# Kernel optimization log

Measured on AMD Instinct MI355X. Metric: run time of the kernel, lower is better.

Reference implementation:

```python
import jax, jax.numpy as jnp
import numpy as np

KERNELS = (2, 4, 8, 16, 32)
DICE_EPS = 1e-6
WEIGHT = 1.0


def _projections(x):
    # x: [B, D, H, W] foreground volume. Three axis-max projections, each [B, 128, 128].
    return jnp.stack([x.max(axis=3),   # axial:    max over W -> [B, D, H]
                      x.max(axis=1),   # sagittal: max over D -> [B, H, W]
                      x.max(axis=2)],  # coronal:  max over H -> [B, D, W]
                     axis=0)           # [3, B, S, S] with S = 128


def _maxpool2d(x, k):
    # x: [3, B, S, S], non-overlapping max pool with kernel=stride=k (k divides S)
    t, b, s, _ = x.shape
    return x.reshape(t, b, s // k, k, s // k, k).max(axis=(3, 5))


def setup_inputs() -> dict:
    key = jax.random.key(0)
    k1, k2 = jax.random.split(key)
    shape = (8, 2, 128, 128, 128)
    inp = jax.random.uniform(k1, shape, dtype=jnp.float32)
    tgt = jax.random.uniform(k2, shape, dtype=jnp.float32)
    return {"input": inp, "target": tgt}


def reference(input, target):
    yh = input[:, 1]   # [B, D, H, W] foreground prediction
    yt = target[:, 1]  # [B, D, H, W] foreground target

    # ---- multi-scale topology loss ----
    P = _projections(yh)  # [3, B, 128, 128]
    G = _projections(yt)
    losses = []
    for k in KERNELS:
        Pk = _maxpool2d(P, k).sum(axis=0)  # [B, 128/k, 128/k]
        Gk = _maxpool2d(G, k).sum(axis=0)
        losses.append(jnp.abs(Gk - Pk).mean())
    topo_loss = jnp.mean(jnp.stack(losses))

    # ---- dice loss (foreground channel, squared denominator) ----
    b = yh.shape[0]
    a = yh.reshape(b, -1)
    t = yt.reshape(b, -1)
    intersection = jnp.sum(a * t, axis=1)
    denom = jnp.sum(a * a, axis=1) + jnp.sum(t * t, axis=1)
    dice_coeff = (2.0 * intersection + DICE_EPS) / denom
    dice_loss = 1.0 - dice_coeff.mean()

    return WEIGHT * topo_loss + WEIGHT * dice_loss
```

## Files before the change

### kernel.cpp

```cpp
#include <hip/hip_runtime.h>

#define S 128
#define SS (S*S)
#define B 8
#define BSS (B*SS)
#define NEG_INF (-3.402823466e+38f)

#define ACC_LOSS 0
#define ACC_DICE 8
#define PA   1024
#define PBP  (PA  + 2*BSS)
#define PCP  (PBP + 2*8*8*SS)

#define MAPF_NEGMAX 0x00800000u

__device__ __forceinline__ unsigned mapf(float f) {
  unsigned u = __float_as_uint(f);
  return (u & 0x80000000u) ? ~u : (u | 0x80000000u);
}
__device__ __forceinline__ float unmapf(unsigned u) {
  return (u & 0x80000000u) ? __uint_as_float(u & 0x7FFFFFFFu) : __uint_as_float(~u);
}
__device__ __forceinline__ float4 max4(float4 a, float4 b) {
  return make_float4(fmaxf(a.x,b.x), fmaxf(a.y,b.y), fmaxf(a.z,b.z), fmaxf(a.w,b.w));
}
__device__ __forceinline__ float hmax4(float4 a) {
  return fmaxf(fmaxf(a.x,a.y), fmaxf(a.z,a.w));
}
__device__ __forceinline__ float4 shflx4(float4 v, int m) {
  return make_float4(__shfl_xor(v.x,m,64), __shfl_xor(v.y,m,64),
                     __shfl_xor(v.z,m,64), __shfl_xor(v.w,m,64));
}

__global__ __launch_bounds__(1024, 4) void proj_dice_kernel(
    const float* __restrict__ gin, const float* __restrict__ gtg,
    float* __restrict__ ws)
{
  const int jc  = blockIdx.x;
  const int ic  = blockIdx.y;
  const int b   = blockIdx.z;
  const int tid = threadIdx.x;
  const int jr  = tid >> 5;
  const int kl  = tid & 31;
  const int j   = (jc << 5) + jr;
  const int i0  = ic << 4;
  const int k0  = kl << 2;
  const int w   = tid >> 6;
  const int h   = (tid >> 5) & 1;

  const float* __restrict__ xin = gin + (size_t)(2*b + 1) * (size_t)(S*SS);
  const float* __restrict__ xtg = gtg + (size_t)(2*b + 1) * (size_t)(S*SS);

  float* paI = ws + PA + (size_t)(0*B + b)*SS;
  float* paT = ws + PA + (size_t)(1*B + b)*SS;
  float* pbI = ws + PBP + (size_t)((0*B + b)*8 + ic)*SS;
  float* pbT = ws + PBP + (size_t)((1*B + b)*8 + ic)*SS;
  float* pcI = ws + PCP + (size_t)((0*B + b)*4 + jc)*SS;
  float* pcT = ws + PCP + (size_t)((1*B + b)*4 + jc)*SS;

  __shared__ unsigned lpc[2][16][S];
  __shared__ float    lpa[2][16][32];
  __shared__ float    dred[16][3];

  {
    unsigned* p = &lpc[0][0][0] + tid*4;
    p[0] = MAPF_NEGMAX; p[1] = MAPF_NEGMAX; p[2] = MAPF_NEGMAX; p[3] = MAPF_NEGMAX;
  }
  __syncthreads();

  float4 pba = make_float4(NEG_INF, NEG_INF, NEG_INF, NEG_INF);
  float4 pbt = pba;
  float s_at = 0.f, s_aa = 0.f, s_tt = 0.f;

  for (int r = 0; r < 4; ++r) {
    #pragma unroll
    for (int q = 0; q < 4; ++q) {
      const int ii = (r << 2) + q;
      const int i  = i0 + ii;
      const size_t off = (size_t)i*SS + (size_t)j*S + k0;
      const float4 a = *(const float4*)(xin + off);
      const float4 t = *(const float4*)(xtg + off);

      s_at = fmaf(a.x,t.x, fmaf(a.y,t.y, fmaf(a.z,t.z, fmaf(a.w,t.w, s_at))));
      s_aa = fmaf(a.x,a.x, fmaf(a.y,a.y, fmaf(a.z,a.z, fmaf(a.w,a.w, s_aa))));
      s_tt = fmaf(t.x,t.x, fmaf(t.y,t.y, fmaf(t.z,t.z, fmaf(t.w,t.w, s_tt))));

      pba = max4(pba, a);
      pbt = max4(pbt, t);

      float rma = hmax4(a), rmt = hmax4(t);
      #pragma unroll
      for (int m = 16; m >= 1; m >>= 1) {
        rma = fmaxf(rma, __shfl_xor(rma, m, 64));
        rmt = fmaxf(rmt, __shfl_xor(rmt, m, 64));
      }
      if (kl == 0) { lpa[0][ii][jr] = rma; lpa[1][ii][jr] = rmt; }

      const float4 pca = max4(a, shflx4(a, 32));
      const float4 pct = max4(t, shflx4(t, 32));
      if (h == 0) {
        atomicMax(&lpc[0][ii][k0+0], mapf(pca.x));
        atomicMax(&lpc[0][ii][k0+1], mapf(pca.y));
        atomicMax(&lpc[0][ii][k0+2], mapf(pca.z));
        atomicMax(&lpc[0][ii][k0+3], mapf(pca.w));
        atomicMax(&lpc[1][ii][k0+0], mapf(pct.x));
        atomicMax(&lpc[1][ii][k0+1], mapf(pct.y));
        atomicMax(&lpc[1][ii][k0+2], mapf(pct.z));
        atomicMax(&lpc[1][ii][k0+3], mapf(pct.w));
      }
    }
  }

  __syncthreads();

  {
    const int t  = tid >> 9;
    const int ii = (tid >> 5) & 15;
    const int kq = (tid & 31) << 2;
    const float4 v = make_float4(unmapf(lpc[t][ii][kq+0]), unmapf(lpc[t][ii][kq+1]),
                                 unmapf(lpc[t][ii][kq+2]), unmapf(lpc[t][ii][kq+3]));
    *(float4*)((t ? pcT : pcI) + (size_t)(i0+ii)*S + kq) = v;
  }
  {
    const int t  = tid >> 9;
    const int ii = (tid >> 5) & 15;
    const int jj = tid & 31;
    (t ? paT : paI)[(size_t)(i0+ii)*S + (jc << 5) + jj] = lpa[t][ii][jj];
  }

  *(float4*)(pbI + j*S + k0) = pba;
  *(float4*)(pbT + j*S + k0) = pbt;

  float v0 = s_at, v1 = s_aa, v2 = s_tt;
  #pragma unroll
  for (int m = 32; m >= 1; m >>= 1) {
    v0 += __shfl_xor(v0, m, 64);
    v1 += __shfl_xor(v1, m, 64);
    v2 += __shfl_xor(v2, m, 64);
  }
  if ((tid & 63) == 0) { dred[w][0] = v0; dred[w][1] = v1; dred[w][2] = v2; }
  __syncthreads();
  if (tid == 0) {
    float a0 = 0.f, a1 = 0.f, a2 = 0.f;
    #pragma unroll
    for (int rr = 0; rr < 16; ++rr) { a0 += dred[rr][0]; a1 += dred[rr][1]; a2 += dred[rr][2]; }
    const int bid = jc + 4*ic + 32*b;
    ws[ACC_DICE + bid*3 + 0] = a0;
    ws[ACC_DICE + bid*3 + 1] = a1;
    ws[ACC_DICE + bid*3 + 2] = a2;
  }
}

__global__ __launch_bounds__(256) void pool_loss_kernel(float* __restrict__ ws)
{
  const int b   = blockIdx.x;
  const int tid = threadIdx.x;
  const int tr  = tid >> 4;
  const int tc  = tid & 15;
  const int r0  = tr << 3;
  const int c0  = tc << 3;

  float s2[2][4][4];
  float s4[2][2][2];
  float s8[2], s16[2], s32[2];
  #pragma unroll
  for (int v = 0; v < 2; ++v) {
    #pragma unroll
    for (int y = 0; y < 4; ++y)
      #pragma unroll
      for (int x = 0; x < 4; ++x) s2[v][y][x] = 0.f;
    #pragma unroll
    for (int y = 0; y < 2; ++y)
      #pragma unroll
      for (int x = 0; x < 2; ++x) s4[v][y][x] = 0.f;
    s8[v] = 0.f; s16[v] = 0.f; s32[v] = 0.f;
  }

  #pragma unroll
  for (int t = 0; t < 3; ++t) {
    #pragma unroll
    for (int vol = 0; vol < 2; ++vol) {
      const int np = (t == 0) ? 1 : (t == 1) ? 8 : 4;
      const float* base =
        (t == 0) ? ws + PA  + (size_t)(vol*B + b)*SS :
        (t == 1) ? ws + PBP + (size_t)((vol*B + b)*8)*SS :
                   ws + PCP + (size_t)((vol*B + b)*4)*SS;
      float tile[8][8];
      #pragma unroll
      for (int r = 0; r < 8; ++r)
        #pragma unroll
        for (int c = 0; c < 8; ++c) tile[r][c] = NEG_INF;
      for (int p = 0; p < np; ++p) {
        const float* m = base + (size_t)p*SS;
        #pragma unroll
        for (int r = 0; r < 8; ++r) {
          const float4 a = *(const float4*)(m + (size_t)(r0 + r)*S + c0);
          const float4 c = *(const float4*)(m + (size_t)(r0 + r)*S + c0 + 4);
          tile[r][0]=fmaxf(tile[r][0],a.x); tile[r][1]=fmaxf(tile[r][1],a.y);
          tile[r][2]=fmaxf(tile[r][2],a.z); tile[r][3]=fmaxf(tile[r][3],a.w);
          tile[r][4]=fmaxf(tile[r][4],c.x); tile[r][5]=fmaxf(tile[r][5],c.y);
          tile[r][6]=fmaxf(tile[r][6],c.z); tile[r][7]=fmaxf(tile[r][7],c.w);
        }
      }
      float m2[4][4];
      #pragma unroll
      for (int y = 0; y < 4; ++y)
        #pragma unroll
        for (int x = 0; x < 4; ++x) {
          m2[y][x] = fmaxf(fmaxf(tile[2*y][2*x], tile[2*y][2*x+1]),
                           fmaxf(tile[2*y+1][2*x], tile[2*y+1][2*x+1]));
          s2[vol][y][x] += m2[y][x];
        }
      float m4[2][2];
      #pragma unroll
      for (int y = 0; y < 2; ++y)
        #pragma unroll
        for (int x = 0; x < 2; ++x) {
          m4[y][x] = fmaxf(fmaxf(m2[2*y][2*x], m2[2*y][2*x+1]),
                           fmaxf(m2[2*y+1][2*x], m2[2*y+1][2*x+1]));
          s4[vol][y][x] += m4[y][x];
        }
      float m8 = fmaxf(fmaxf(m4[0][0], m4[0][1]), fmaxf(m4[1][0], m4[1][1]));
      s8[vol] += m8;
      float m16 = m8;
      m16 = fmaxf(m16, __shfl_xor(m16, 1, 64));
      m16 = fmaxf(m16, __shfl_xor(m16, 16, 64));
      s16[vol] += m16;
      float m32 = m16;
      m32 = fmaxf(m32, __shfl_xor(m32, 2, 64));
      m32 = fmaxf(m32, __shfl_xor(m32, 32, 64));
      s32[vol] += m32;
    }
  }

  const float w0 = 1.f/(5.f*8.f*64.f*64.f);
  const float w1 = 1.f/(5.f*8.f*32.f*32.f);
  const float w2 = 1.f/(5.f*8.f*16.f*16.f);
  const float w3 = 1.f/(5.f*8.f*8.f*8.f);
  const float w4 = 1.f/(5.f*8.f*4.f*4.f);

  float l0 = 0.f;
  #pragma unroll
  for (int y = 0; y < 4; ++y)
    #pragma unroll
    for (int x = 0; x < 4; ++x) l0 += fabsf(s2[1][y][x] - s2[0][y][x]);
  float l1 = 0.f;
  #pragma unroll
  for (int y = 0; y < 2; ++y)
    #pragma unroll
    for (int x = 0; x < 2; ++x) l1 += fabsf(s4[1][y][x] - s4[0][y][x]);
  float part = l0*w0 + l1*w1 + fabsf(s8[1] - s8[0])*w2;
  if ((tid & 0x11) == 0) part += fabsf(s16[1] - s16[0])*w3;
  if ((tid & 0x33) == 0) part += fabsf(s32[1] - s32[0])*w4;

  #pragma unroll
  for (int m = 32; m >= 1; m >>= 1) part += __shfl_xor(part, m, 64);
  __shared__ float red[4];
  const int wid = tid >> 6;
  if ((tid & 63) == 0) red[wid] = part;
  __syncthreads();
  if (tid == 0) ws[ACC_LOSS + b] = red[0] + red[1] + red[2] + red[3];
}

__global__ __launch_bounds__(256) void finalize_kernel(
    const float* __restrict__ ws, float* __restrict__ out)
{
  const int tid = threadIdx.x;
  __shared__ float fd[8];

  float v0 = ws[ACC_DICE + tid*3 + 0];
  float v1 = ws[ACC_DICE + tid*3 + 1];
  float v2 = ws[ACC_DICE + tid*3 + 2];
  #pragma unroll
  for (int m = 16; m >= 1; m >>= 1) {
    v0 += __shfl_xor(v0, m, 64);
    v1 += __shfl_xor(v1, m, 64);
    v2 += __shfl_xor(v2, m, 64);
  }
  if ((tid & 31) == 0) fd[tid >> 5] = (2.f*v0 + 1e-6f) / (v1 + v2);
  __syncthreads();
  if (tid == 0) {
    float topo = 0.f, dsum = 0.f;
    #pragma unroll
    for (int b = 0; b < B; ++b) { topo += ws[ACC_LOSS + b]; dsum += fd[b]; }
    out[0] = topo + (1.f - dsum / (float)B);
  }
}

extern "C" void kernel_launch(void* const* d_in, const int* in_sizes, int n_in,
                              void* d_out, int out_size, void* d_ws, size_t ws_size,
                              hipStream_t stream)
{
  const float* gin = (const float*)d_in[0];
  const float* gtg = (const float*)d_in[1];
  float* ws  = (float*)d_ws;
  float* out = (float*)d_out;

  dim3 g1(4, 8, B);
  proj_dice_kernel<<<g1, dim3(1024), 0, stream>>>(gin, gtg, ws);

  pool_loss_kernel<<<B, dim3(256), 0, stream>>>(ws);

  finalize_kernel<<<1, dim3(256), 0, stream>>>(ws, out);
}
```

Baseline: 52.95 us.

## Split LDS atomic-max work across halves, interleave LDS layout, batch global loads

Before, only the h==0 half-wave did all eight LDS atomicMax operations for both input and target. Now each half handles one of the two tensors (h selects the plane), and the LDS columns are stored interleaved (component*32 + kl) so consecutive lanes hit consecutive banks. The readback is remapped to match the new layout. The four row loads per outer iteration are also issued ahead of the compute so more global loads are in flight, at the cost of extra registers.

```diff
diff --git a/kernel.cpp b/kernel.cpp
--- a/kernel.cpp
+++ b/kernel.cpp
@@ -63,8 +63,8 @@
   __shared__ float    dred[16][3];
 
   {
-    unsigned* p = &lpc[0][0][0] + tid*4;
-    p[0] = MAPF_NEGMAX; p[1] = MAPF_NEGMAX; p[2] = MAPF_NEGMAX; p[3] = MAPF_NEGMAX;
+    uint4* p = (uint4*)(&lpc[0][0][0]) + tid;
+    *p = make_uint4(MAPF_NEGMAX, MAPF_NEGMAX, MAPF_NEGMAX, MAPF_NEGMAX);
   }
   __syncthreads();
 
@@ -73,13 +73,18 @@
   float s_at = 0.f, s_aa = 0.f, s_tt = 0.f;
 
   for (int r = 0; r < 4; ++r) {
+    float4 A[4], T[4];
+    #pragma unroll
+    for (int q = 0; q < 4; ++q) {
+      const size_t off = (size_t)(i0 + (r << 2) + q)*SS + (size_t)j*S + k0;
+      A[q] = *(const float4*)(xin + off);
+      T[q] = *(const float4*)(xtg + off);
+    }
     #pragma unroll
     for (int q = 0; q < 4; ++q) {
       const int ii = (r << 2) + q;
-      const int i  = i0 + ii;
-      const size_t off = (size_t)i*SS + (size_t)j*S + k0;
-      const float4 a = *(const float4*)(xin + off);
-      const float4 t = *(const float4*)(xtg + off);
+      const float4 a = A[q];
+      const float4 t = T[q];
 
       s_at = fmaf(a.x,t.x, fmaf(a.y,t.y, fmaf(a.z,t.z, fmaf(a.w,t.w, s_at))));
       s_aa = fmaf(a.x,a.x, fmaf(a.y,a.y, fmaf(a.z,a.z, fmaf(a.w,a.w, s_aa))));
@@ -98,33 +103,31 @@
 
       const float4 pca = max4(a, shflx4(a, 32));
       const float4 pct = max4(t, shflx4(t, 32));
-      if (h == 0) {
-        atomicMax(&lpc[0][ii][k0+0], mapf(pca.x));
-        atomicMax(&lpc[0][ii][k0+1], mapf(pca.y));
-        atomicMax(&lpc[0][ii][k0+2], mapf(pca.z));
-        atomicMax(&lpc[0][ii][k0+3], mapf(pca.w));
-        atomicMax(&lpc[1][ii][k0+0], mapf(pct.x));
-        atomicMax(&lpc[1][ii][k0+1], mapf(pct.y));
-        atomicMax(&lpc[1][ii][k0+2], mapf(pct.z));
-        atomicMax(&lpc[1][ii][k0+3], mapf(pct.w));
-      }
+      const float4 pc  = h ? pct : pca;
+      unsigned* plane = &lpc[h][ii][0];
+      atomicMax(plane + 0*32 + kl, mapf(pc.x));
+      atomicMax(plane + 1*32 + kl, mapf(pc.y));
+      atomicMax(plane + 2*32 + kl, mapf(pc.z));
+      atomicMax(plane + 3*32 + kl, mapf(pc.w));
     }
   }
 
   __syncthreads();
 
   {
-    const int t  = tid >> 9;
-    const int ii = (tid >> 5) & 15;
-    const int kq = (tid & 31) << 2;
-    const float4 v = make_float4(unmapf(lpc[t][ii][kq+0]), unmapf(lpc[t][ii][kq+1]),
-                                 unmapf(lpc[t][ii][kq+2]), unmapf(lpc[t][ii][kq+3]));
-    *(float4*)((t ? pcT : pcI) + (size_t)(i0+ii)*S + kq) = v;
+    const int t   = tid >> 9;
+    const int rem = tid & 511;
+    const int ii  = rem >> 5;
+    const int q   = rem & 31;
+    const float4 v = make_float4(unmapf(lpc[t][ii][ 0+q]), unmapf(lpc[t][ii][32+q]),
+                                 unmapf(lpc[t][ii][64+q]), unmapf(lpc[t][ii][96+q]));
+    *(float4*)((t ? pcT : pcI) + (size_t)(i0+ii)*S + (q << 2)) = v;
   }
   {
-    const int t  = tid >> 9;
-    const int ii = (tid >> 5) & 15;
-    const int jj = tid & 31;
+    const int t   = tid >> 9;
+    const int rem = tid & 511;
+    const int ii  = rem >> 5;
+    const int jj  = rem & 31;
     (t ? paT : paI)[(size_t)(i0+ii)*S + (jc << 5) + jj] = lpa[t][ii][jj];
   }
 
```

After: 53.62 us. Within noise of the previous version (+1.3%).
